# Performance work log

Measured on AMD Instinct MI355X. Metric: run time of the kernel, lower is better.

The kernel has to match this reference:

```python
import jax, jax.numpy as jnp
import numpy as np

B, H, W = 2, 512, 512
C2, HEADS = 128, 8
EPS_NORM = 1e-12  # torch F.normalize eps


def conv2d(x, w, groups=1):
    # x: NCHW, w: OIHW, stride 1, SAME padding
    return jax.lax.conv_general_dilated(
        x, w, window_strides=(1, 1), padding='SAME',
        dimension_numbers=('NCHW', 'OIHW', 'NCHW'),
        feature_group_count=groups)


def setup_inputs() -> dict:
    key = jax.random.key(0)
    ks = jax.random.split(key, 7)
    x = jax.random.normal(ks[0], (B, 2, H, W), dtype=jnp.float32)
    e = jax.random.normal(ks[1], (B, 1, H, W), dtype=jnp.float32)
    # imhead: 1x1 conv 2 -> 2*C2, then 3x3 depthwise conv on 2*C2 channels
    w_conv1 = jax.random.normal(ks[2], (2 * C2, 2, 1, 1), dtype=jnp.float32) * 0.5
    w_dw = jax.random.normal(ks[3], (2 * C2, 1, 3, 3), dtype=jnp.float32) * 0.2
    # ehead: 3x3 conv 1 -> C2 (groups=1)
    w_ehead = jax.random.normal(ks[4], (C2, 1, 3, 3), dtype=jnp.float32) * 0.2
    # project_out: 1x1 conv C2 -> 2
    w_proj = jax.random.normal(ks[5], (2, C2, 1, 1), dtype=jnp.float32) * 0.1
    a1 = jnp.ones((HEADS, 1, 1), dtype=jnp.float32)
    return {"x": x, "e": e, "w_conv1": w_conv1, "w_dw": w_dw,
            "w_ehead": w_ehead, "w_proj": w_proj, "a1": a1}


def l2norm_lastdim(t):
    n = jnp.sqrt(jnp.sum(t * t, axis=-1, keepdims=True))
    return t / jnp.maximum(n, EPS_NORM)


def reference(x, e, w_conv1, w_dw, w_ehead, w_proj, a1):
    b, _, h, w = x.shape
    # NOTE: attHead_image.forward never applies its LayerNorm, so neither do we.
    q1 = conv2d(x, w_conv1)                 # (B, 2*C2, H, W)
    q1 = conv2d(q1, w_dw, groups=2 * C2)    # depthwise 3x3
    k_eg = conv2d(e, w_ehead)               # (B, C2, H, W)
    q_im, v_im = jnp.split(q1, 2, axis=1)   # each (B, C2, H, W)

    def heads(t):  # (B, C2, H, W) -> (B, head, c, H*W)
        return t.reshape(b, HEADS, C2 // HEADS, h * w)

    q = l2norm_lastdim(heads(q_im))
    k = l2norm_lastdim(heads(k_eg))
    v = heads(v_im)

    # channel-wise attention: (B, head, c, c)
    attn = jnp.einsum('bhcn,bhdn->bhcd', q, k) * a1
    attn = jax.nn.softmax(attn, axis=-1)
    out = jnp.einsum('bhcd,bhdn->bhcn', attn, v)  # (B, head, c, H*W)
    out = out.reshape(b, C2, h, w)
    return x + conv2d(out, w_proj)
```

## Files before the change

### kernel.cpp

```cpp
#include <hip/hip_runtime.h>

#define IMG 512
#define NPIX (IMG*IMG)

__global__ __launch_bounds__(256,2) void gram_kernel(const float* __restrict__ x,
                                                     const float* __restrict__ e,
                                                     float* __restrict__ part){
  const int dyi = blockIdx.y;
  const int dy  = dyi - 2;
  const int b   = blockIdx.z;
  const int col = ((blockIdx.x & 1) << 8) | threadIdx.x;
  const int r0  = (blockIdx.x >> 1) << 4;
  const float* x0 = x + (size_t)b*2*NPIX;
  const float* x1 = x0 + NPIX;
  const float* ep = e + (size_t)b*NPIX;

  float acc[6][5];
#pragma unroll
  for (int t=0;t<6;t++)
#pragma unroll
    for (int j=0;j<5;j++) acc[t][j]=0.f;

#pragma unroll 4
  for (int s=0;s<16;s++){
    const int r = r0+s;
    const float a0 = x0[r*IMG+col];
    const float a1v= x1[r*IMG+col];
    const float aE = ep[r*IMG+col];
    const int rb = r+dy;
    if ((unsigned)rb < (unsigned)IMG){
      const float* p0 = x0 + rb*IMG;
      const float* p1 = x1 + rb*IMG;
      const float* pe = ep + rb*IMG;
#pragma unroll
      for (int j=0;j<5;j++){
        const int cc = col-2+j;
        const bool ok = (unsigned)cc < (unsigned)IMG;
        const float b0 = ok ? p0[cc] : 0.f;
        const float b1 = ok ? p1[cc] : 0.f;
        const float be = ok ? pe[cc] : 0.f;
        acc[0][j] += a0 *b0;
        acc[1][j] += a0 *b1;
        acc[2][j] += a1v*b1;
        acc[3][j] += a0 *be;
        acc[4][j] += a1v*be;
        acc[5][j] += aE *be;
      }
    }
  }

  __shared__ float red[4][30];
  const int wv   = threadIdx.x >> 6;
  const int lane = threadIdx.x & 63;
#pragma unroll
  for (int t=0;t<6;t++)
#pragma unroll
    for (int j=0;j<5;j++){
      float v = acc[t][j];
      for (int off=32; off; off>>=1) v += __shfl_down(v, off);
      if (lane==0) red[wv][t*5+j] = v;
    }
  __syncthreads();
  if (threadIdx.x < 30){
    const int g = b*5 + dyi;
    part[(size_t)((g*64)+blockIdx.x)*32 + threadIdx.x] =
      red[0][threadIdx.x]+red[1][threadIdx.x]+red[2][threadIdx.x]+red[3][threadIdx.x];
  }
}

__global__ __launch_bounds__(256,1) void attn_kernel(const float* __restrict__ part,
                                                     const float* __restrict__ w_conv1,
                                                     const float* __restrict__ w_dw,
                                                     const float* __restrict__ w_ehead,
                                                     const float* __restrict__ w_proj,
                                                     const float* __restrict__ a1,
                                                     float* __restrict__ AB){
  const int tid = threadIdx.x;
  __shared__ float Lred[2][150];
  __shared__ float we_lds[128][9];
  __shared__ float nk_lds[2][128];
  __shared__ float attn_lds[2][8][16][16];
  __shared__ float M_lds[2][2][128];

  for (int i=tid; i<300; i+=256){
    const int bb=i/150, li=i%150;
    const int t=li/25, lag=li%25, dyi=lag/5, dxi=lag%5;
    const int g = bb*5+dyi;
    const float* p = part + (size_t)(g*64)*32 + t*5+dxi;
    float s=0.f;
    for (int j=0;j<64;j++) s += p[j*32];
    Lred[bb][li]=s;
  }
  if (tid<128){
#pragma unroll
    for (int t=0;t<9;t++) we_lds[tid][t]=w_ehead[tid*9+t];
  }
  __syncthreads();

  const int b=tid>>7, h=(tid>>4)&7, c=tid&15;
  const int C=h*16+c;
  const float* Lb  = Lred[b];
  const float* L00=Lb, *L01=Lb+25, *L11=Lb+50, *L0e=Lb+75, *L1e=Lb+100, *Lee=Lb+125;

  float u[9], v[9];
  {
    const float wa=w_conv1[C*2+0], wb=w_conv1[C*2+1];
#pragma unroll
    for (int t=0;t<9;t++){ const float wd=w_dw[C*9+t]; u[t]=wd*wa; v[t]=wd*wb; }
  }
  float nq2=0.f, nk2=0.f;
#pragma unroll
  for (int t=0;t<9;t++){
    const int ty=t/3, tx=t%3;
#pragma unroll
    for (int t2=0;t2<9;t2++){
      const int dy=t2/3-ty, dx=t2%3-tx;
      const int di=( dy+2)*5+( dx+2);
      const int dj=(-dy+2)*5+(-dx+2);
      nq2 += u[t]*u[t2]*L00[di] + u[t]*v[t2]*L01[di] + v[t]*u[t2]*L01[dj] + v[t]*v[t2]*L11[di];
      nk2 += we_lds[C][t]*we_lds[C][t2]*Lee[di];
    }
  }
  nk_lds[b][C]=sqrtf(nk2);
  float P[9];
#pragma unroll
  for (int t2=0;t2<9;t2++){
    float s=0.f;
    const int t2y=t2/3, t2x=t2%3;
#pragma unroll
    for (int t=0;t<9;t++){
      const int di=(t2y-t/3+2)*5+(t2x-t%3+2);
      s += u[t]*L0e[di] + v[t]*L1e[di];
    }
    P[t2]=s;
  }
  __syncthreads();
  const float inv_nq = 1.f/fmaxf(sqrtf(nq2), 1e-12f);
  const float a1h=a1[h];
  float lg[16], mx=-1e30f;
#pragma unroll
  for (int d=0; d<16; d++){
    float S=0.f;
#pragma unroll
    for (int t2=0;t2<9;t2++) S += P[t2]*we_lds[h*16+d][t2];
    const float l = S*inv_nq/fmaxf(nk_lds[b][h*16+d],1e-12f)*a1h;
    lg[d]=l; mx=fmaxf(mx,l);
  }
  float sum=0.f;
#pragma unroll
  for (int d=0;d<16;d++){ lg[d]=expf(lg[d]-mx); sum+=lg[d]; }
  const float inv=1.f/sum;
#pragma unroll
  for (int d=0;d<16;d++) attn_lds[b][h][c][d]=lg[d]*inv;
  __syncthreads();
  for (int i=tid;i<512;i+=256){
    const int G=i&127, o=(i>>7)&1, bb=i>>8;
    const int hh=G>>4, dd=G&15;
    float s=0.f;
#pragma unroll
    for (int cc=0;cc<16;cc++) s += w_proj[o*128 + hh*16+cc]*attn_lds[bb][hh][cc][dd];
    M_lds[bb][o][G]=s;
  }
  __syncthreads();
  if (tid<36){
    const int t=tid%9, o=(tid/9)&1, bb=tid/18;
    float sa=0.f, sb=0.f;
    for (int G=0;G<128;G++){
      const float m=M_lds[bb][o][G];
      const float wd=w_dw[(128+G)*9+t];
      sa += m*wd*w_conv1[(128+G)*2+0];
      sb += m*wd*w_conv1[(128+G)*2+1];
    }
    AB[(bb*2+o)*9+t]      = sa;
    AB[72 + (bb*2+o)*9+t] = sb;
  }
}

__global__ __launch_bounds__(256,1) void out_kernel(const float* __restrict__ x,
                                                    const float* __restrict__ AB,
                                                    float* __restrict__ out){
  const int idx = blockIdx.x*256 + threadIdx.x;
  const int b  = idx >> 16;
  const int y  = (idx >> 7) & (IMG-1);
  const int xc = (idx & 127) << 2;
  const float* x0 = x + (size_t)b*2*NPIX;
  const float* x1 = x0 + NPIX;

  float A0[9],A1[9],B0[9],B1[9];
#pragma unroll
  for (int t=0;t<9;t++){
    A0[t]=AB[(b*2+0)*9+t];      A1[t]=AB[(b*2+1)*9+t];
    B0[t]=AB[72+(b*2+0)*9+t];   B1[t]=AB[72+(b*2+1)*9+t];
  }
  float v0[3][6], v1[3][6];
#pragma unroll
  for (int r=0;r<3;r++){
    const int yy=y-1+r;
    if ((unsigned)yy < (unsigned)IMG){
      const float* p0=x0+(size_t)yy*IMG;
      const float* p1=x1+(size_t)yy*IMG;
      const float4 m0=*(const float4*)(p0+xc);
      const float4 m1=*(const float4*)(p1+xc);
      v0[r][1]=m0.x; v0[r][2]=m0.y; v0[r][3]=m0.z; v0[r][4]=m0.w;
      v1[r][1]=m1.x; v1[r][2]=m1.y; v1[r][3]=m1.z; v1[r][4]=m1.w;
      v0[r][0]=(xc>0)?p0[xc-1]:0.f;        v1[r][0]=(xc>0)?p1[xc-1]:0.f;
      v0[r][5]=(xc+4<IMG)?p0[xc+4]:0.f;    v1[r][5]=(xc+4<IMG)?p1[xc+4]:0.f;
    } else {
#pragma unroll
      for (int c2=0;c2<6;c2++){v0[r][c2]=0.f;v1[r][c2]=0.f;}
    }
  }
  float res0[4], res1[4];
#pragma unroll
  for (int i=0;i<4;i++){
    float s0=v0[1][i+1];
    float s1=v1[1][i+1];
#pragma unroll
    for (int t=0;t<9;t++){
      const int ty=t/3, tx=t%3;
      const float g0=v0[ty][i+tx], g1=v1[ty][i+tx];
      s0 += A0[t]*g0 + B0[t]*g1;
      s1 += A1[t]*g0 + B1[t]*g1;
    }
    res0[i]=s0; res1[i]=s1;
  }
  float* o0p = out + ((size_t)(b*2+0)*IMG + y)*IMG + xc;
  float* o1p = out + ((size_t)(b*2+1)*IMG + y)*IMG + xc;
  *(float4*)o0p = make_float4(res0[0],res0[1],res0[2],res0[3]);
  *(float4*)o1p = make_float4(res1[0],res1[1],res1[2],res1[3]);
}

extern "C" void kernel_launch(void* const* d_in, const int* in_sizes, int n_in,
                              void* d_out, int out_size, void* d_ws, size_t ws_size,
                              hipStream_t stream){
  const float* x       = (const float*)d_in[0];
  const float* e       = (const float*)d_in[1];
  const float* w_conv1 = (const float*)d_in[2];
  const float* w_dw    = (const float*)d_in[3];
  const float* w_ehead = (const float*)d_in[4];
  const float* w_proj  = (const float*)d_in[5];
  const float* a1      = (const float*)d_in[6];
  float* ws   = (float*)d_ws;
  float* part = ws;
  float* AB   = ws + 20480;
  float* out  = (float*)d_out;

  hipLaunchKernelGGL(gram_kernel, dim3(64,5,2), dim3(256), 0, stream, x, e, part);
  hipLaunchKernelGGL(attn_kernel, dim3(1),      dim3(256), 0, stream, part,
                     w_conv1, w_dw, w_ehead, w_proj, a1, AB);
  hipLaunchKernelGGL(out_kernel,  dim3(512),    dim3(256), 0, stream, x, AB, out);
}
```

Measured before the change: 43.62 us.

## Vectorize gram kernel with float4 columns and halve block count

Each thread in the gram kernel now handles four adjacent columns using float4 loads. It builds an 8-wide window of the shifted row from three float4 loads per channel, so neighbouring lag products reuse registers instead of issuing five scalar loads each. Each block covers 16 rows split into two halves of 8, so the grid and the partial-sum buffer shrink by half and the attn kernel reduction now loops over 32 partials. This cuts load instruction count and redundant neighbour loads, at the cost of more registers per thread and fewer blocks to hide latency.

```diff
diff --git a/kernel.cpp b/kernel.cpp
--- a/kernel.cpp
+++ b/kernel.cpp
@@ -9,8 +9,9 @@
   const int dyi = blockIdx.y;
   const int dy  = dyi - 2;
   const int b   = blockIdx.z;
-  const int col = ((blockIdx.x & 1) << 8) | threadIdx.x;
-  const int r0  = (blockIdx.x >> 1) << 4;
+  const int half= threadIdx.x >> 7;
+  const int cx  = (threadIdx.x & 127) << 2;
+  const int r0  = (blockIdx.x << 4) + (half << 3);
   const float* x0 = x + (size_t)b*2*NPIX;
   const float* x1 = x0 + NPIX;
   const float* ep = e + (size_t)b*NPIX;
@@ -21,30 +22,44 @@
 #pragma unroll
     for (int j=0;j<5;j++) acc[t][j]=0.f;
 
-#pragma unroll 4
-  for (int s=0;s<16;s++){
+  const bool okL = (cx >= 4), okR = (cx < 508);
+
+#pragma unroll 2
+  for (int s=0;s<8;s++){
     const int r = r0+s;
-    const float a0 = x0[r*IMG+col];
-    const float a1v= x1[r*IMG+col];
-    const float aE = ep[r*IMG+col];
+    const float4 a0 = *(const float4*)(x0 + r*IMG + cx);
+    const float4 a1 = *(const float4*)(x1 + r*IMG + cx);
+    const float4 aE = *(const float4*)(ep + r*IMG + cx);
     const int rb = r+dy;
     if ((unsigned)rb < (unsigned)IMG){
       const float* p0 = x0 + rb*IMG;
       const float* p1 = x1 + rb*IMG;
       const float* pe = ep + rb*IMG;
+      float w0[8], w1[8], wE[8];
+      {
+        const float4 z = make_float4(0.f,0.f,0.f,0.f);
+        float4 L,M,R;
+        L = okL ? *(const float4*)(p0+cx-4) : z;
+        M = *(const float4*)(p0+cx);
+        R = okR ? *(const float4*)(p0+cx+4) : z;
+        w0[0]=L.z;w0[1]=L.w;w0[2]=M.x;w0[3]=M.y;w0[4]=M.z;w0[5]=M.w;w0[6]=R.x;w0[7]=R.y;
+        L = okL ? *(const float4*)(p1+cx-4) : z;
+        M = *(const float4*)(p1+cx);
+        R = okR ? *(const float4*)(p1+cx+4) : z;
+        w1[0]=L.z;w1[1]=L.w;w1[2]=M.x;w1[3]=M.y;w1[4]=M.z;w1[5]=M.w;w1[6]=R.x;w1[7]=R.y;
+        L = okL ? *(const float4*)(pe+cx-4) : z;
+        M = *(const float4*)(pe+cx);
+        R = okR ? *(const float4*)(pe+cx+4) : z;
+        wE[0]=L.z;wE[1]=L.w;wE[2]=M.x;wE[3]=M.y;wE[4]=M.z;wE[5]=M.w;wE[6]=R.x;wE[7]=R.y;
+      }
 #pragma unroll
       for (int j=0;j<5;j++){
-        const int cc = col-2+j;
-        const bool ok = (unsigned)cc < (unsigned)IMG;
-        const float b0 = ok ? p0[cc] : 0.f;
-        const float b1 = ok ? p1[cc] : 0.f;
-        const float be = ok ? pe[cc] : 0.f;
-        acc[0][j] += a0 *b0;
-        acc[1][j] += a0 *b1;
-        acc[2][j] += a1v*b1;
-        acc[3][j] += a0 *be;
-        acc[4][j] += a1v*be;
-        acc[5][j] += aE *be;
+        acc[0][j] += a0.x*w0[j] + a0.y*w0[j+1] + a0.z*w0[j+2] + a0.w*w0[j+3];
+        acc[1][j] += a0.x*w1[j] + a0.y*w1[j+1] + a0.z*w1[j+2] + a0.w*w1[j+3];
+        acc[2][j] += a1.x*w1[j] + a1.y*w1[j+1] + a1.z*w1[j+2] + a1.w*w1[j+3];
+        acc[3][j] += a0.x*wE[j] + a0.y*wE[j+1] + a0.z*wE[j+2] + a0.w*wE[j+3];
+        acc[4][j] += a1.x*wE[j] + a1.y*wE[j+1] + a1.z*wE[j+2] + a1.w*wE[j+3];
+        acc[5][j] += aE.x*wE[j] + aE.y*wE[j+1] + aE.z*wE[j+2] + aE.w*wE[j+3];
       }
     }
   }
@@ -63,7 +78,7 @@
   __syncthreads();
   if (threadIdx.x < 30){
     const int g = b*5 + dyi;
-    part[(size_t)((g*64)+blockIdx.x)*32 + threadIdx.x] =
+    part[(size_t)((g*32)+blockIdx.x)*32 + threadIdx.x] =
       red[0][threadIdx.x]+red[1][threadIdx.x]+red[2][threadIdx.x]+red[3][threadIdx.x];
   }
 }
@@ -86,9 +101,10 @@
     const int bb=i/150, li=i%150;
     const int t=li/25, lag=li%25, dyi=lag/5, dxi=lag%5;
     const int g = bb*5+dyi;
-    const float* p = part + (size_t)(g*64)*32 + t*5+dxi;
+    const float* p = part + (size_t)(g*32)*32 + t*5+dxi;
     float s=0.f;
-    for (int j=0;j<64;j++) s += p[j*32];
+#pragma unroll
+    for (int j=0;j<32;j++) s += p[j*32];
     Lred[bb][li]=s;
   }
   if (tid<128){
@@ -242,10 +258,10 @@
   const float* a1      = (const float*)d_in[6];
   float* ws   = (float*)d_ws;
   float* part = ws;
-  float* AB   = ws + 20480;
+  float* AB   = ws + 10240;
   float* out  = (float*)d_out;
 
-  hipLaunchKernelGGL(gram_kernel, dim3(64,5,2), dim3(256), 0, stream, x, e, part);
+  hipLaunchKernelGGL(gram_kernel, dim3(32,5,2), dim3(256), 0, stream, x, e, part);
   hipLaunchKernelGGL(attn_kernel, dim3(1),      dim3(256), 0, stream, part,
                      w_conv1, w_dw, w_ehead, w_proj, a1, AB);
   hipLaunchKernelGGL(out_kernel,  dim3(512),    dim3(256), 0, stream, x, AB, out);
```

Measured after the change: 44.82 us. 2.8% more time.
